# Performance work log

Measured on AMD Instinct MI355X. Metric: run time of the kernel, lower is better.

The kernel has to match this reference:

```python
import jax, jax.numpy as jnp
import numpy as np

V, E, H, HC = 20000, 300, 512, 256
B, N, LE, NW, LW, NC, LC = 16, 64, 16, 8, 16, 64, 16


def _gru_dir(xg, W_hh, b_hh, reverse):
    # xg: [B, T, 3*Hc] precomputed input gates; returns final hidden [B, Hc]
    xs = jnp.swapaxes(xg, 0, 1)
    if reverse:
        xs = xs[::-1]
    h0 = jnp.zeros((xg.shape[0], W_hh.shape[1]), xg.dtype)

    def step(h, xt):
        hr, hz, hn = jnp.split(h @ W_hh.T + b_hh, 3, axis=-1)
        xr, xz, xn = jnp.split(xt, 3, axis=-1)
        r = jax.nn.sigmoid(xr + hr)
        z = jax.nn.sigmoid(xz + hz)
        n = jnp.tanh(xn + r * hn)
        return (1.0 - z) * n + z * h, None

    hT, _ = jax.lax.scan(step, h0, xs)
    return hT


def _bigru(x, Wif, Whf, bif, bhf, Wib, Whb, bib, bhb):
    # x: [B, T, D] -> concat(fwd final, bwd final) = [B, 2*Hc]  (matches torch h_n.permute(1,0,2).reshape)
    hf = _gru_dir(x @ Wif.T + bif, Whf, bhf, False)
    hb = _gru_dir(x @ Wib.T + bib, Whb, bhb, True)
    return jnp.concatenate([hf, hb], axis=-1)


def setup_inputs() -> dict:
    key = jax.random.key(0)
    ks = iter(jax.random.split(key, 64))
    f = lambda *s: jax.random.normal(next(ks), s, jnp.float32) * 0.05
    ri = lambda *s: jax.random.randint(next(ks), s, 0, V)
    return {
        "emb_table": f(V, E),
        "W_prj": f(H, E),
        "dn_Wif": f(3 * HC, H), "dn_Whf": f(3 * HC, HC), "dn_bif": f(3 * HC), "dn_bhf": f(3 * HC),
        "dn_Wib": f(3 * HC, H), "dn_Whb": f(3 * HC, HC), "dn_bib": f(3 * HC), "dn_bhb": f(3 * HC),
        "W_e": f(H, H), "W_l": f(H, H), "W_w": f(H, H),
        "Wg": f(H, H), "bg": f(H),
        "diff_Wif": f(3 * H, H), "diff_Whf": f(3 * H, H), "diff_bif": f(3 * H), "diff_bhf": f(3 * H),
        "diff_Wib": f(3 * H, H), "diff_Whb": f(3 * H, H), "diff_bib": f(3 * H), "diff_bhb": f(3 * H),
        "Wc": f(1, 2 * H), "bc": f(1),
        "Wa1": f(2 * H, 2 * H), "ba1": f(2 * H), "Wa2": f(1, 2 * H), "ba2": f(1),
        "local_adj": jnp.zeros((64, 64), jnp.float32),
        "obs": ri(B, 32),
        "local_graph": ri(64, 8),
        "entities": ri(B, N, LE),
        "locals_": ri(B, N, LE),
        "worlds": ri(B, N, NW, LW),
        "commands": ri(B, NC, LC),
    }


def reference(emb_table, W_prj,
              dn_Wif, dn_Whf, dn_bif, dn_bhf, dn_Wib, dn_Whb, dn_bib, dn_bhb,
              W_e, W_l, W_w, Wg, bg,
              diff_Wif, diff_Whf, diff_bif, diff_bhf, diff_Wib, diff_Whb, diff_bib, diff_bhb,
              Wc, bc, Wa1, ba1, Wa2, ba2,
              local_adj, obs, local_graph, entities, locals_, worlds, commands):
    dn = (dn_Wif, dn_Whf, dn_bif, dn_bhf, dn_Wib, dn_Whb, dn_bib, dn_bhb)
    emb = lambda ids: emb_table[ids] @ W_prj.T  # embedding lookup + no-bias projection to H

    b, n, le = entities.shape
    ent_h = _bigru(emb(entities).reshape(b * n, le, H), *dn).reshape(b, n, H)
    ll = locals_.shape[-1]
    loc_h = _bigru(emb(locals_).reshape(b * n, ll, H), *dn).reshape(b, n, H)
    nw, lw = worlds.shape[2], worlds.shape[3]
    w_h = _bigru(emb(worlds).reshape(b * n * nw, lw, H), *dn).reshape(b, n, nw, H)
    worlds_sum = (w_h @ W_w).sum(axis=2)  # [b, n, H]

    # torch.ones(H,H) + W_e  ==  broadcastable 1.0 + W_e
    graph_hidden = jax.nn.elu(ent_h @ (1.0 + W_e)) + jax.nn.elu(loc_h @ W_l) + worlds_sum
    graph_encoding = jax.nn.elu(jax.nn.elu(graph_hidden) @ Wg.T + bg)  # graph_prj (dropout=eval identity)

    # value network: 'diff' path
    diff_h = _bigru(graph_encoding, diff_Wif, diff_Whf, diff_bif, diff_bhf,
                    diff_Wib, diff_Whb, diff_bib, diff_bhb)  # [b, 2H]
    value = (diff_h @ Wc.T + bc).reshape(b, 1, 1)

    nc, lc = commands.shape[1], commands.shape[2]
    c_h = _bigru(emb(commands).reshape(b * nc, lc, H), *dn).reshape(b, nc, H)

    rep = jnp.concatenate([
        jnp.broadcast_to(c_h[:, None, :, :], (b, n, nc, H)),
        jnp.broadcast_to(graph_encoding[:, :, None, :], (b, n, nc, H)),
    ], axis=-1)  # [b, n, nc, 2H]
    s = jax.nn.elu(rep @ Wa1.T + ba1) @ Wa2.T + ba2  # att_cmd (dropout p=0)
    scores = s[..., 0].mean(axis=1)  # mean over entities -> [b, nc]

    mask = commands.sum(axis=2) > 0
    probs = jax.nn.softmax(jnp.where(mask, scores, -1e9), axis=1)
    index = jnp.argmax(probs, axis=1).reshape(1, b, 1)  # deterministic stand-in for multinomial(1)
    return scores, index, value
```

## Files before the change

kernel.cpp:

```cpp
#include <hip/hip_runtime.h>
#include <stdint.h>

#define DEVFN __device__ __forceinline__

typedef __attribute__((ext_vector_type(4))) float fx4;
typedef __attribute__((ext_vector_type(8))) short sx8;
typedef __bf16 bf16x8 __attribute__((ext_vector_type(8)));

DEVFN float eluf(float x){ return x>0.f ? x : __expf(x)-1.f; }
DEVFN float sigm(float x){ return 1.f/(1.f+__expf(-x)); }
DEVFN float tanhf_(float x){ float cx=fminf(10.f,fmaxf(-10.f,x)); float e=__expf(-2.f*cx); return (1.f-e)/(1.f+e); }

DEVFN fx4 MFMA(sx8 a, sx8 b, fx4 c){
  return __builtin_amdgcn_mfma_f32_16x16x32_bf16(
      __builtin_bit_cast(bf16x8,a), __builtin_bit_cast(bf16x8,b), c, 0,0,0);
}
DEVFN void splitf(float x, short& hi, short& lo){
  __bf16 h = (__bf16)x; hi = __builtin_bit_cast(short, h);
  __bf16 l = (__bf16)(x - (float)h); lo = __builtin_bit_cast(short, l);
}

struct TT { const float* src; float* dst; int srows, scols, drows; };
struct TTs { TT t[4]; };
__global__ void k_prep_t(TTs ts){
  TT tk = ts.t[blockIdx.y];
  size_t tot = (size_t)tk.drows * tk.srows;
  for (size_t i = (size_t)blockIdx.x*256 + threadIdx.x; i < tot; i += (size_t)gridDim.x*256){
    int c = (int)(i / tk.srows), r = (int)(i % tk.srows);
    tk.dst[i] = (c < tk.scols) ? tk.src[(size_t)r*tk.scols + c] : 0.f;
  }
}
struct PL { const float* src; __bf16* hi; __bf16* lo; size_t n; };
struct PLs { PL t[2]; };
__global__ void k_prep_planes(PLs ts){
  PL tk = ts.t[blockIdx.y];
  for (size_t i = (size_t)blockIdx.x*256 + threadIdx.x; i < tk.n; i += (size_t)gridDim.x*256){
    float x = tk.src[i];
    __bf16 h = (__bf16)x;
    tk.hi[i] = h; tk.lo[i] = (__bf16)(x - (float)h);
  }
}
struct BC { const float* src; __bf16* dst; size_t n; };
struct BCs { BC t[2]; };
__global__ void k_prep_b16(BCs ts){
  BC tk = ts.t[blockIdx.y];
  for (size_t i = (size_t)blockIdx.x*256 + threadIdx.x; i < tk.n; i += (size_t)gridDim.x*256)
    tk.dst[i] = (__bf16)tk.src[i];
}
__global__ void k_toks(const int* __restrict__ ents, const int* __restrict__ locs,
                       const int* __restrict__ wrl, const int* __restrict__ cmd,
                       int* __restrict__ toks){
  int idx = blockIdx.x*256 + threadIdx.x;
  if (idx >= 2*16*11264) return;
  int dir = idx / (16*11264);
  int rem = idx % (16*11264);
  int s = rem / 11264, c = rem % 11264;
  const int* tp;
  if (c<1024) tp = ents + c*16;
  else if (c<2048) tp = locs + (c-1024)*16;
  else if (c<10240) tp = wrl + (c-2048)*16;
  else tp = cmd + (c-10240)*16;
  toks[idx] = tp[dir ? 15-s : s];
}
__global__ void k_cat_bias(const float* __restrict__ a, const float* __restrict__ b,
                           float* __restrict__ o){
  int i = blockIdx.x*256 + threadIdx.x;
  if (i < 768) o[i] = a[i];
  else if (i < 1536) o[i] = b[i-768];
}

template<int EPI, int OBF>
__global__ __launch_bounds__(256) void gemm_k(
    const float* __restrict__ A, const float* __restrict__ B,
    const float* __restrict__ bias, void* __restrict__ out,
    int M, int N, int Kpad, int Kreal, int lda, int ldb)
{
  int bm = blockIdx.y*64, bn = blockIdx.x*64;
  int tid = threadIdx.x, l = tid&63, w = tid>>6;
  int wm = (w>>1)*32, wn = (w&1)*32;
  int lr = l&15, lk = l>>4;
  fx4 acc[2][2] = {};
  for (int k0 = 0; k0 < Kpad; k0 += 32) {
    sx8 ahi[2], alo[2], bhi[2], blo[2];
    bool full = (k0 + 32 <= Kreal);
    #pragma unroll
    for (int i=0;i<2;i++){
      int row = bm + wm + i*16 + lr; row = row < M ? row : M-1;
      int col = bn + wn + i*16 + lr;
      const float* ap = A + (size_t)row*lda + k0 + lk*8;
      const float* bp = B + (size_t)col*ldb + k0 + lk*8;
      float av[8], bv[8];
      if (full){
        *(fx4*)av = *(const fx4*)ap; *(fx4*)(av+4) = *(const fx4*)(ap+4);
        *(fx4*)bv = *(const fx4*)bp; *(fx4*)(bv+4) = *(const fx4*)(bp+4);
      } else {
        #pragma unroll
        for (int j=0;j<8;j++){
          int k = k0 + lk*8 + j;
          av[j] = (k < Kreal) ? ap[j] : 0.f;
          bv[j] = (k < Kreal) ? bp[j] : 0.f;
        }
      }
      #pragma unroll
      for (int j=0;j<8;j++){
        short h,lo2; splitf(av[j], h, lo2); ahi[i][j]=h; alo[i][j]=lo2;
        splitf(bv[j], h, lo2); bhi[i][j]=h; blo[i][j]=lo2;
      }
    }
    #pragma unroll
    for (int i=0;i<2;i++)
      #pragma unroll
      for (int j=0;j<2;j++){
        acc[i][j] = MFMA(alo[i], bhi[j], acc[i][j]);
        acc[i][j] = MFMA(ahi[i], blo[j], acc[i][j]);
        acc[i][j] = MFMA(ahi[i], bhi[j], acc[i][j]);
      }
  }
  #pragma unroll
  for (int i=0;i<2;i++)
    #pragma unroll
    for (int j=0;j<2;j++)
      #pragma unroll
      for (int q=0;q<4;q++){
        int m = bm + wm + i*16 + lk*4 + q;
        int n = bn + wn + j*16 + lr;
        if (m < M){
          float v = acc[i][j][q];
          if (EPI>=1) v += bias[n];
          if (EPI==2) v = eluf(v);
          if (OBF) ((__bf16*)out)[(size_t)m*N + n] = (__bf16)v;
          else     ((float*)out)[(size_t)m*N + n] = v;
        }
      }
}

struct DnDir {
  const __bf16 *Hshi, *Hslo;
  __bf16 *Hdhi, *Hdlo;
  const __bf16 *Whi, *Wlo;
  const float *bias;
  const float *T;
  const int *toks;
  int tstride;
  int dircol;
};
__global__ __launch_bounds__(512) void dn_step(DnDir d0, DnDir d1,
                                               float* __restrict__ seqh, int s)
{
  int bx = blockIdx.x;
  int sel = (bx >= 176) ? 1 : 0;
  DnDir d = sel ? d1 : d0;
  int bm = (bx - sel*176)*64;
  int jbase = blockIdx.y*128;
  int tid = threadIdx.x, l = tid&63, w = tid>>6;
  int mg = (w>>2)*32;
  int jq = (w&3)*32;
  int lr = l&15, lk = l>>4;
  fx4 acc[2][2][3] = {};
  if (s > 0){
    for (int kk=0;kk<8;kk++){
      sx8 ah[2], al[2];
      #pragma unroll
      for (int i=0;i<2;i++){
        int m = bm + mg + i*16 + lr;
        ah[i] = *(const sx8*)(d.Hshi + (size_t)m*256 + kk*32 + lk*8);
        al[i] = *(const sx8*)(d.Hslo + (size_t)m*256 + kk*32 + lk*8);
      }
      #pragma unroll
      for (int jt=0;jt<2;jt++){
        #pragma unroll
        for (int role=0;role<3;role++){
          int col = role*256 + jbase + jq + jt*16 + lr;
          sx8 bhf = *(const sx8*)(d.Whi + (size_t)col*256 + kk*32 + lk*8);
          sx8 blf = *(const sx8*)(d.Wlo + (size_t)col*256 + kk*32 + lk*8);
          #pragma unroll
          for (int i=0;i<2;i++){
            fx4 a = acc[i][jt][role];
            a = MFMA(al[i], bhf, a);
            a = MFMA(ah[i], blf, a);
            a = MFMA(ah[i], bhf, a);
            acc[i][jt][role] = a;
          }
        }
      }
    }
  }
  const int* tks = d.toks + s*11264;
  #pragma unroll
  for (int i=0;i<2;i++){
    #pragma unroll
    for (int q=0;q<4;q++){
      int m = bm + mg + i*16 + lk*4 + q;
      int tok = tks[m];
      const float* trow = d.T + (size_t)tok*d.tstride;
      #pragma unroll
      for (int jt=0;jt<2;jt++){
        int j = jbase + jq + jt*16 + lr;
        float hr = acc[i][jt][0][q] + d.bias[j];
        float hz = acc[i][jt][1][q] + d.bias[256+j];
        float hn = acc[i][jt][2][q] + d.bias[512+j];
        float xr = trow[j], xz = trow[256+j], xn = trow[512+j];
        float ho = 0.f;
        if (s > 0) ho = (float)d.Hshi[(size_t)m*256+j] + (float)d.Hslo[(size_t)m*256+j];
        float r = sigm(xr+hr), z = sigm(xz+hz);
        float n = tanhf_(xn + r*hn);
        float v = (1.f-z)*n + z*ho;
        __bf16 hh = (__bf16)v;
        d.Hdhi[(size_t)m*256+j] = hh;
        d.Hdlo[(size_t)m*256+j] = (__bf16)(v - (float)hh);
        if (s == 15) seqh[(size_t)m*512 + d.dircol*256 + j] = v;
      }
    }
  }
}

__global__ void k_wsum(const float* __restrict__ seqh, float* __restrict__ ws){
  int r = blockIdx.x;
  for (int c = threadIdx.x; c < 512; c += 256){
    float a = 0.f;
    #pragma unroll
    for (int w8=0; w8<8; w8++) a += seqh[((size_t)2048 + r*8 + w8)*512 + c];
    ws[(size_t)r*512 + c] = a;
  }
}
__global__ void k_rowsum(const float* __restrict__ seqh, float* __restrict__ rs){
  int r = blockIdx.x, l = threadIdx.x;
  float a = 0.f;
  for (int c=l;c<512;c+=64) a += seqh[(size_t)r*512+c];
  #pragma unroll
  for (int o=32;o>0;o>>=1) a += __shfl_down(a,o);
  if (l==0) rs[r]=a;
}
__global__ void k_combine(const float* __restrict__ E1, const float* __restrict__ E2,
                          const float* __restrict__ E3, const float* __restrict__ rs,
                          float* __restrict__ y){
  size_t i = (size_t)blockIdx.x*256 + threadIdx.x;
  int r = (int)(i >> 9);
  float g = eluf(E1[i] + rs[r]) + eluf(E2[i]) + E3[i];
  y[i] = eluf(g);
}

__global__ __launch_bounds__(256) void diff_step(
  const float* __restrict__ hsrc, float* __restrict__ hdst,
  const __bf16* __restrict__ Whf, const __bf16* __restrict__ Whb,
  const float* __restrict__ bhf, const float* __restrict__ bhb,
  const __bf16* __restrict__ Xf, const __bf16* __restrict__ Xb, int t)
{
  int wg = blockIdx.x;
  int dir = wg>>3, seg = wg&7;
  const __bf16* W = dir? Whb: Whf;
  const float* bh = dir? bhb: bhf;
  const __bf16* X = dir? Xb: Xf;
  int tt = dir? 63-t : t;
  int tid = threadIdx.x, l = tid&63, w = tid>>6;
  int lr=l&15, lk=l>>4;
  int jbase = seg*64 + w*16;
  fx4 acc[3] = {};
  const float* hrow = hsrc + (size_t)dir*16*512;
  for (int kk=0;kk<16;kk++){
    const float* ap = hrow + (size_t)lr*512 + kk*32 + lk*8;
    float av[8];
    *(fx4*)av = *(const fx4*)ap; *(fx4*)(av+4) = *(const fx4*)(ap+4);
    sx8 ah, al;
    #pragma unroll
    for (int j=0;j<8;j++){ short h,lo; splitf(av[j],h,lo); ah[j]=h; al[j]=lo; }
    #pragma unroll
    for (int role=0;role<3;role++){
      int col = role*512 + jbase + lr;
      sx8 b = *(const sx8*)(W + (size_t)col*512 + kk*32 + lk*8);
      acc[role] = MFMA(al, b, acc[role]);
      acc[role] = MFMA(ah, b, acc[role]);
    }
  }
  #pragma unroll
  for (int q=0;q<4;q++){
    int m = lk*4+q;
    int j = jbase + lr;
    float hr = acc[0][q] + bh[j];
    float hz = acc[1][q] + bh[512+j];
    float hn = acc[2][q] + bh[1024+j];
    const __bf16* xrow = X + ((size_t)m*64 + tt)*1536;
    float xr = (float)xrow[j], xz = (float)xrow[512+j], xn = (float)xrow[1024+j];
    float ho = hrow[(size_t)m*512 + j];
    float r = sigm(xr+hr), z = sigm(xz+hz);
    float n = tanhf_(xn + r*hn);
    hdst[((size_t)dir*16 + m)*512 + j] = (1.f-z)*n + z*ho;
  }
}

__global__ __launch_bounds__(256) void k_score(
  const float* __restrict__ Amat, const float* __restrict__ Gmat,
  const float* __restrict__ Wa2, const float* __restrict__ ba2, float* __restrict__ sc)
{
  __shared__ float red[4];
  int p = blockIdx.x, b = p>>6, tid = threadIdx.x;
  float av[4], wv[4];
  #pragma unroll
  for (int k=0;k<4;k++){ av[k] = Amat[(size_t)p*1024 + tid + k*256]; wv[k] = Wa2[tid + k*256]; }
  float acc = 0.f;
  for (int n=0;n<64;n++){
    const float* g = Gmat + ((size_t)b*64+n)*1024;
    #pragma unroll
    for (int k=0;k<4;k++) acc += wv[k]*eluf(av[k] + g[tid + k*256]);
  }
  #pragma unroll
  for (int o=32;o>0;o>>=1) acc += __shfl_down(acc,o);
  if ((tid&63)==0) red[tid>>6] = acc;
  __syncthreads();
  if (tid==0) sc[p] = (red[0]+red[1]+red[2]+red[3])*(1.f/64.f) + ba2[0];
}

__global__ void k_final(const float* __restrict__ sc, const int* __restrict__ cmds,
                        const float* __restrict__ hfin, const float* __restrict__ Wc,
                        const float* __restrict__ bc, float* __restrict__ out)
{
  int b = blockIdx.x, l = threadIdx.x;
  out[b*64+l] = sc[b*64+l];
  int ssum = 0;
  const int* cr = cmds + (b*64+l)*16;
  #pragma unroll
  for (int k=0;k<16;k++) ssum += cr[k];
  float v = ssum>0 ? sc[b*64+l] : -1e9f;
  int idx = l;
  #pragma unroll
  for (int o=32;o>0;o>>=1){
    float ov = __shfl_down(v,o); int oi = __shfl_down(idx,o);
    if (ov > v || (ov==v && oi<idx)) { v=ov; idx=oi; }
  }
  if (l==0) out[1024 + b] = (float)idx;
  float a = 0.f;
  for (int j=l;j<512;j+=64) a += hfin[(size_t)b*512+j] * Wc[j];
  for (int j=l;j<512;j+=64) a += hfin[(size_t)(16+b)*512+j] * Wc[512+j];
  #pragma unroll
  for (int o=32;o>0;o>>=1) a += __shfl_down(a,o);
  if (l==0) out[1040 + b] = a + bc[0];
}

static inline void launch_gemm(hipStream_t st, const float* A, const float* B,
                               const float* bias, void* out, int M, int N,
                               int Kpad, int Kreal, int lda, int ldb, int epi, int obf)
{
  dim3 g(N/64, (M+63)/64), blk(256);
  if      (epi==0 && obf==0) gemm_k<0,0><<<g,blk,0,st>>>(A,B,bias,out,M,N,Kpad,Kreal,lda,ldb);
  else if (epi==1 && obf==0) gemm_k<1,0><<<g,blk,0,st>>>(A,B,bias,out,M,N,Kpad,Kreal,lda,ldb);
  else if (epi==2 && obf==0) gemm_k<2,0><<<g,blk,0,st>>>(A,B,bias,out,M,N,Kpad,Kreal,lda,ldb);
  else                       gemm_k<1,1><<<g,blk,0,st>>>(A,B,bias,out,M,N,Kpad,Kreal,lda,ldb);
}

extern "C" void kernel_launch(void* const* d_in, const int* in_sizes, int n_in,
                              void* d_out, int out_size, void* d_ws, size_t ws_size,
                              hipStream_t stream) {
  (void)in_sizes; (void)n_in; (void)out_size;
  const float* emb   = (const float*)d_in[0];
  const float* W_prj = (const float*)d_in[1];
  const float* dnWif = (const float*)d_in[2];
  const float* dnWhf = (const float*)d_in[3];
  const float* dnbif = (const float*)d_in[4];
  const float* dnbhf = (const float*)d_in[5];
  const float* dnWib = (const float*)d_in[6];
  const float* dnWhb = (const float*)d_in[7];
  const float* dnbib = (const float*)d_in[8];
  const float* dnbhb = (const float*)d_in[9];
  const float* W_e   = (const float*)d_in[10];
  const float* W_l   = (const float*)d_in[11];
  const float* W_w   = (const float*)d_in[12];
  const float* Wg    = (const float*)d_in[13];
  const float* bg    = (const float*)d_in[14];
  const float* dWif  = (const float*)d_in[15];
  const float* dWhf  = (const float*)d_in[16];
  const float* dbif  = (const float*)d_in[17];
  const float* dbhf  = (const float*)d_in[18];
  const float* dWib  = (const float*)d_in[19];
  const float* dWhb  = (const float*)d_in[20];
  const float* dbib  = (const float*)d_in[21];
  const float* dbhb  = (const float*)d_in[22];
  const float* Wc    = (const float*)d_in[23];
  const float* bc    = (const float*)d_in[24];
  const float* Wa1   = (const float*)d_in[25];
  const float* ba1   = (const float*)d_in[26];
  const float* Wa2   = (const float*)d_in[27];
  const float* ba2   = (const float*)d_in[28];
  const int* ents = (const int*)d_in[32];
  const int* locs = (const int*)d_in[33];
  const int* wrl  = (const int*)d_in[34];
  const int* cmds = (const int*)d_in[35];

  char* ws = (char*)d_ws;
  size_t off = 0;
#define WSP(name, type, count) type* name = (type*)(ws + off); off += (((size_t)(count))*sizeof(type) + 255) & ~(size_t)255;
  WSP(pWprjT, float, 320*512);
  WSP(pC2,    float, 1536*320);
  WSP(pB2,    float, 1536);
  WSP(pWhFhi, __bf16, 768*256);
  WSP(pWhFlo, __bf16, 768*256);
  WSP(pWhBhi, __bf16, 768*256);
  WSP(pWhBlo, __bf16, 768*256);
  WSP(pWeT,   float, 512*512);
  WSP(pWlT,   float, 512*512);
  WSP(pWwT,   float, 512*512);
  WSP(pdWhF,  __bf16, 1536*512);
  WSP(pdWhB,  __bf16, 1536*512);
  WSP(pSeqh,  float, 11264*512);
  WSP(pH0hi,  __bf16, 11264*256);
  WSP(pH0lo,  __bf16, 11264*256);
  WSP(pH1hi,  __bf16, 11264*256);
  WSP(pH1lo,  __bf16, 11264*256);
  WSP(pH2A,   __bf16, 11264*256);
  WSP(pH2B,   __bf16, 11264*256);
  WSP(pH2C,   __bf16, 11264*256);
  WSP(pH2D,   __bf16, 11264*256);
  WSP(pToks,  int,    2*16*11264);
  WSP(pHA,    float, 32*512);
  WSP(pHB,    float, 32*512);
  WSP(pRs,    float, 1024);
  WSP(pScf,   float, 1024);
#undef WSP
  __bf16* pH2hi[2] = { pH2A, pH2C };
  __bf16* pH2lo[2] = { pH2B, pH2D };
  float* pT = (float*)(ws + off);
  size_t trem = (ws_size > off) ? (ws_size - off) : 0;
  const size_t TBL = (size_t)20000*1536*sizeof(float);
  bool comb = trem >= TBL;

  const size_t SZ = (size_t)1024*512*4;
  char* sc = (char*)pT;
  float* pWsum = (float*)(sc + 0*SZ);
  float* pE1   = (float*)(sc + 1*SZ);
  float* pE2   = (float*)(sc + 2*SZ);
  float* pE3   = (float*)(sc + 3*SZ);
  float* pY    = (float*)(sc + 4*SZ);
  float* pGe   = (float*)(sc + 5*SZ);
  float* pAmat = (float*)(sc + 6*SZ);
  float* pGmat = (float*)(sc + 8*SZ);
  __bf16* pXf  = (__bf16*)(sc + 10*SZ);
  __bf16* pXb  = (__bf16*)(sc + 10*SZ + (size_t)1024*1536*2);

  TTs tt;
  tt.t[0] = { W_prj, pWprjT, 512, 300, 320 };
  tt.t[1] = { W_e,   pWeT,   512, 512, 512 };
  tt.t[2] = { W_l,   pWlT,   512, 512, 512 };
  tt.t[3] = { W_w,   pWwT,   512, 512, 512 };
  k_prep_t<<<dim3(256,4), 256, 0, stream>>>(tt);
  PLs pl;
  pl.t[0] = { dnWhf, pWhFhi, pWhFlo, (size_t)768*256 };
  pl.t[1] = { dnWhb, pWhBhi, pWhBlo, (size_t)768*256 };
  k_prep_planes<<<dim3(256,2), 256, 0, stream>>>(pl);
  BCs bcs;
  bcs.t[0] = { dWhf, pdWhF, (size_t)1536*512 };
  bcs.t[1] = { dWhb, pdWhB, (size_t)1536*512 };
  k_prep_b16<<<dim3(512,2), 256, 0, stream>>>(bcs);
  k_toks<<<1408, 256, 0, stream>>>(ents, locs, wrl, cmds, pToks);
  k_cat_bias<<<6, 256, 0, stream>>>(dnbif, dnbib, pB2);

  launch_gemm(stream, dnWif, pWprjT, nullptr, pC2,           768, 320, 512, 512, 512, 512, 0, 0);
  launch_gemm(stream, dnWib, pWprjT, nullptr, pC2 + 768*320, 768, 320, 512, 512, 512, 512, 0, 0);

  if (comb){
    launch_gemm(stream, emb, pC2, pB2, pT, 20000, 1536, 320, 300, 300, 320, 1, 0);
    for (int s = 0; s < 16; ++s){
      int pp = s & 1;
      DnDir D0 = { pp? pH1hi:pH0hi, pp? pH1lo:pH0lo,
                   pp? pH0hi:pH1hi, pp? pH0lo:pH1lo,
                   pWhFhi, pWhFlo, dnbhf, pT,       pToks,               1536, 0 };
      DnDir D1 = { pH2hi[pp], pH2lo[pp], pH2hi[pp^1], pH2lo[pp^1],
                   pWhBhi, pWhBlo, dnbhb, pT + 768, pToks + 16*11264,    1536, 1 };
      dn_step<<<dim3(352,2), 512, 0, stream>>>(D0, D1, pSeqh, s);
    }
  } else {
    for (int dir = 0; dir < 2; ++dir){
      launch_gemm(stream, emb, dir? pC2 + 768*320 : pC2, dir? dnbib : dnbif, pT,
                  20000, 768, 320, 300, 300, 320, 1, 0);
      for (int s = 0; s < 16; ++s){
        int pp = s & 1;
        DnDir D = { pp? pH1hi:pH0hi, pp? pH1lo:pH0lo,
                    pp? pH0hi:pH1hi, pp? pH0lo:pH1lo,
                    dir? pWhBhi:pWhFhi, dir? pWhBlo:pWhFlo, dir? dnbhb:dnbhf,
                    pT, pToks + (size_t)dir*16*11264, 768, dir };
        dn_step<<<dim3(176,2), 512, 0, stream>>>(D, D, pSeqh, s);
      }
    }
  }

  k_wsum<<<1024, 256, 0, stream>>>(pSeqh, pWsum);
  k_rowsum<<<1024, 64, 0, stream>>>(pSeqh, pRs);
  launch_gemm(stream, pSeqh,                   pWeT, nullptr, pE1, 1024, 512, 512, 512, 512, 512, 0, 0);
  launch_gemm(stream, pSeqh + (size_t)1024*512,pWlT, nullptr, pE2, 1024, 512, 512, 512, 512, 512, 0, 0);
  launch_gemm(stream, pWsum,                   pWwT, nullptr, pE3, 1024, 512, 512, 512, 512, 512, 0, 0);
  k_combine<<<2048, 256, 0, stream>>>(pE1, pE2, pE3, pRs, pY);
  launch_gemm(stream, pY, Wg, bg, pGe, 1024, 512, 512, 512, 512, 512, 2, 0);
  launch_gemm(stream, pGe, dWif, dbif, pXf, 1024, 1536, 512, 512, 512, 512, 1, 1);
  launch_gemm(stream, pGe, dWib, dbib, pXb, 1024, 1536, 512, 512, 512, 512, 1, 1);
  launch_gemm(stream, pSeqh + (size_t)10240*512, Wa1, nullptr, pAmat, 1024, 1024, 512, 512, 512, 1024, 0, 0);
  launch_gemm(stream, pGe, Wa1 + 512, ba1, pGmat, 1024, 1024, 512, 512, 512, 1024, 1, 0);
  k_score<<<1024, 256, 0, stream>>>(pAmat, pGmat, Wa2, ba2, pScf);
  hipMemsetAsync(pHA, 0, 32*512*sizeof(float), stream);
  float* ha = pHA; float* hb = pHB;
  for (int t=0; t<64; ++t){
    diff_step<<<16, 256, 0, stream>>>(ha, hb, pdWhF, pdWhB, dbhf, dbhb, pXf, pXb, t);
    float* tmp = ha; ha = hb; hb = tmp;
  }
  k_final<<<16, 64, 0, stream>>>(pScf, cmds, ha, Wc, bc, (float*)d_out);
}
```

Baseline: 2.965 ms.

## Fuse per-token input projection into GRU step instead of precomputing vocab table

Drops the precomputed 20000x1536 gate table (a full-vocab GEMM that most tokens never use). Instead, each recurrent step gathers the bf16 hi/lo split embeddings for its tokens and multiplies them by the folded projection on the fly with MFMA. Tiles now cover 32 rows by all 256 hidden columns per block, and workspace buffers get fixed allocations. This adds per-step input GEMM work (10 k-iterations of 3-pass MFMA) across the 16 sequential steps, in exchange for removing the large table GEMM and its memory traffic.

```diff
diff --git a/kernel.cpp b/kernel.cpp
--- a/kernel.cpp
+++ b/kernel.cpp
@@ -38,6 +38,16 @@
     float x = tk.src[i];
     __bf16 h = (__bf16)x;
     tk.hi[i] = h; tk.lo[i] = (__bf16)(x - (float)h);
+  }
+}
+__global__ void k_split(const float* __restrict__ src, __bf16* __restrict__ hi,
+                        __bf16* __restrict__ lo, int rows, int cin, int cout, int stride){
+  size_t tot = (size_t)rows * cout;
+  for (size_t i = (size_t)blockIdx.x*256 + threadIdx.x; i < tot; i += (size_t)gridDim.x*256){
+    int r = (int)(i / cout), c = (int)(i % cout);
+    float x = (c < cin) ? src[(size_t)r*stride + c] : 0.f;
+    __bf16 h = (__bf16)x;
+    hi[i] = h; lo[i] = (__bf16)(x - (float)h);
   }
 }
 struct BC { const float* src; __bf16* dst; size_t n; };
@@ -134,35 +144,64 @@
       }
 }
 
-struct DnDir {
+struct DnD {
   const __bf16 *Hshi, *Hslo;
   __bf16 *Hdhi, *Hdlo;
   const __bf16 *Whi, *Wlo;
-  const float *bias;
-  const float *T;
+  const __bf16 *Chi, *Clo;
+  const float *bH, *bX;
+  const __bf16 *Ehi, *Elo;
   const int *toks;
-  int tstride;
   int dircol;
 };
-__global__ __launch_bounds__(512) void dn_step(DnDir d0, DnDir d1,
+__global__ __launch_bounds__(512) void dn_step(DnD d0, DnD d1,
                                                float* __restrict__ seqh, int s)
 {
   int bx = blockIdx.x;
-  int sel = (bx >= 176) ? 1 : 0;
-  DnDir d = sel ? d1 : d0;
-  int bm = (bx - sel*176)*64;
-  int jbase = blockIdx.y*128;
+  int sel = (bx >= 352) ? 1 : 0;
+  DnD d = sel ? d1 : d0;
+  int cb = (bx - sel*352)*32;
   int tid = threadIdx.x, l = tid&63, w = tid>>6;
-  int mg = (w>>2)*32;
-  int jq = (w&3)*32;
+  int jq = w*32;
   int lr = l&15, lk = l>>4;
-  fx4 acc[2][2][3] = {};
+  const int* tks = d.toks + s*11264;
+  int tokA[2];
+  tokA[0] = tks[cb + lr];
+  tokA[1] = tks[cb + 16 + lr];
+  fx4 aRZ[2][2][2] = {};
+  fx4 aHn[2][2] = {};
+  fx4 aXn[2][2] = {};
+  for (int kk=0; kk<10; ++kk){
+    sx8 eh[2], el[2];
+    #pragma unroll
+    for (int i=0;i<2;i++){
+      eh[i] = *(const sx8*)(d.Ehi + (size_t)tokA[i]*320 + kk*32 + lk*8);
+      el[i] = *(const sx8*)(d.Elo + (size_t)tokA[i]*320 + kk*32 + lk*8);
+    }
+    #pragma unroll
+    for (int jt=0;jt<2;jt++){
+      #pragma unroll
+      for (int role=0;role<3;role++){
+        int col = role*256 + jq + jt*16 + lr;
+        sx8 bh_ = *(const sx8*)(d.Chi + (size_t)col*320 + kk*32 + lk*8);
+        sx8 bl_ = *(const sx8*)(d.Clo + (size_t)col*320 + kk*32 + lk*8);
+        #pragma unroll
+        for (int i=0;i<2;i++){
+          fx4 a = (role<2) ? aRZ[i][jt][role] : aXn[i][jt];
+          a = MFMA(el[i], bh_, a);
+          a = MFMA(eh[i], bl_, a);
+          a = MFMA(eh[i], bh_, a);
+          if (role<2) aRZ[i][jt][role] = a; else aXn[i][jt] = a;
+        }
+      }
+    }
+  }
   if (s > 0){
     for (int kk=0;kk<8;kk++){
       sx8 ah[2], al[2];
       #pragma unroll
       for (int i=0;i<2;i++){
-        int m = bm + mg + i*16 + lr;
+        int m = cb + i*16 + lr;
         ah[i] = *(const sx8*)(d.Hshi + (size_t)m*256 + kk*32 + lk*8);
         al[i] = *(const sx8*)(d.Hslo + (size_t)m*256 + kk*32 + lk*8);
       }
@@ -170,39 +209,35 @@
       for (int jt=0;jt<2;jt++){
         #pragma unroll
         for (int role=0;role<3;role++){
-          int col = role*256 + jbase + jq + jt*16 + lr;
-          sx8 bhf = *(const sx8*)(d.Whi + (size_t)col*256 + kk*32 + lk*8);
-          sx8 blf = *(const sx8*)(d.Wlo + (size_t)col*256 + kk*32 + lk*8);
+          int col = role*256 + jq + jt*16 + lr;
+          sx8 bh_ = *(const sx8*)(d.Whi + (size_t)col*256 + kk*32 + lk*8);
+          sx8 bl_ = *(const sx8*)(d.Wlo + (size_t)col*256 + kk*32 + lk*8);
           #pragma unroll
           for (int i=0;i<2;i++){
-            fx4 a = acc[i][jt][role];
-            a = MFMA(al[i], bhf, a);
-            a = MFMA(ah[i], blf, a);
-            a = MFMA(ah[i], bhf, a);
-            acc[i][jt][role] = a;
+            fx4 a = (role<2) ? aRZ[i][jt][role] : aHn[i][jt];
+            a = MFMA(al[i], bh_, a);
+            a = MFMA(ah[i], bl_, a);
+            a = MFMA(ah[i], bh_, a);
+            if (role<2) aRZ[i][jt][role] = a; else aHn[i][jt] = a;
           }
         }
       }
     }
   }
-  const int* tks = d.toks + s*11264;
   #pragma unroll
   for (int i=0;i<2;i++){
     #pragma unroll
     for (int q=0;q<4;q++){
-      int m = bm + mg + i*16 + lk*4 + q;
-      int tok = tks[m];
-      const float* trow = d.T + (size_t)tok*d.tstride;
+      int m = cb + i*16 + lk*4 + q;
       #pragma unroll
       for (int jt=0;jt<2;jt++){
-        int j = jbase + jq + jt*16 + lr;
-        float hr = acc[i][jt][0][q] + d.bias[j];
-        float hz = acc[i][jt][1][q] + d.bias[256+j];
-        float hn = acc[i][jt][2][q] + d.bias[512+j];
-        float xr = trow[j], xz = trow[256+j], xn = trow[512+j];
+        int j = jq + jt*16 + lr;
+        float r = sigm(aRZ[i][jt][0][q] + d.bX[j]     + d.bH[j]);
+        float z = sigm(aRZ[i][jt][1][q] + d.bX[256+j] + d.bH[256+j]);
+        float xn = aXn[i][jt][q] + d.bX[512+j];
+        float hn = aHn[i][jt][q] + d.bH[512+j];
         float ho = 0.f;
         if (s > 0) ho = (float)d.Hshi[(size_t)m*256+j] + (float)d.Hslo[(size_t)m*256+j];
-        float r = sigm(xr+hr), z = sigm(xz+hz);
         float n = tanhf_(xn + r*hn);
         float v = (1.f-z)*n + z*ho;
         __bf16 hh = (__bf16)v;
@@ -350,7 +385,7 @@
 extern "C" void kernel_launch(void* const* d_in, const int* in_sizes, int n_in,
                               void* d_out, int out_size, void* d_ws, size_t ws_size,
                               hipStream_t stream) {
-  (void)in_sizes; (void)n_in; (void)out_size;
+  (void)in_sizes; (void)n_in; (void)out_size; (void)ws_size;
   const float* emb   = (const float*)d_in[0];
   const float* W_prj = (const float*)d_in[1];
   const float* dnWif = (const float*)d_in[2];
@@ -391,6 +426,10 @@
   WSP(pWprjT, float, 320*512);
   WSP(pC2,    float, 1536*320);
   WSP(pB2,    float, 1536);
+  WSP(pEhi,   __bf16, 20000*320);
+  WSP(pElo,   __bf16, 20000*320);
+  WSP(pC2hi,  __bf16, 1536*320);
+  WSP(pC2lo,  __bf16, 1536*320);
   WSP(pWhFhi, __bf16, 768*256);
   WSP(pWhFlo, __bf16, 768*256);
   WSP(pWhBhi, __bf16, 768*256);
@@ -414,26 +453,19 @@
   WSP(pHB,    float, 32*512);
   WSP(pRs,    float, 1024);
   WSP(pScf,   float, 1024);
+  WSP(pWsum,  float, 1024*512);
+  WSP(pE1,    float, 1024*512);
+  WSP(pE2,    float, 1024*512);
+  WSP(pE3,    float, 1024*512);
+  WSP(pY,     float, 1024*512);
+  WSP(pGe,    float, 1024*512);
+  WSP(pAmat,  float, 1024*1024);
+  WSP(pGmat,  float, 1024*1024);
+  WSP(pXf,    __bf16, 1024*1536);
+  WSP(pXb,    __bf16, 1024*1536);
 #undef WSP
   __bf16* pH2hi[2] = { pH2A, pH2C };
   __bf16* pH2lo[2] = { pH2B, pH2D };
-  float* pT = (float*)(ws + off);
-  size_t trem = (ws_size > off) ? (ws_size - off) : 0;
-  const size_t TBL = (size_t)20000*1536*sizeof(float);
-  bool comb = trem >= TBL;
-
-  const size_t SZ = (size_t)1024*512*4;
-  char* sc = (char*)pT;
-  float* pWsum = (float*)(sc + 0*SZ);
-  float* pE1   = (float*)(sc + 1*SZ);
-  float* pE2   = (float*)(sc + 2*SZ);
-  float* pE3   = (float*)(sc + 3*SZ);
-  float* pY    = (float*)(sc + 4*SZ);
-  float* pGe   = (float*)(sc + 5*SZ);
-  float* pAmat = (float*)(sc + 6*SZ);
-  float* pGmat = (float*)(sc + 8*SZ);
-  __bf16* pXf  = (__bf16*)(sc + 10*SZ);
-  __bf16* pXb  = (__bf16*)(sc + 10*SZ + (size_t)1024*1536*2);
 
   TTs tt;
   tt.t[0] = { W_prj, pWprjT, 512, 300, 320 };
@@ -451,34 +483,22 @@
   k_prep_b16<<<dim3(512,2), 256, 0, stream>>>(bcs);
   k_toks<<<1408, 256, 0, stream>>>(ents, locs, wrl, cmds, pToks);
   k_cat_bias<<<6, 256, 0, stream>>>(dnbif, dnbib, pB2);
+  k_split<<<2048, 256, 0, stream>>>(emb, pEhi, pElo, 20000, 300, 320, 300);
 
   launch_gemm(stream, dnWif, pWprjT, nullptr, pC2,           768, 320, 512, 512, 512, 512, 0, 0);
   launch_gemm(stream, dnWib, pWprjT, nullptr, pC2 + 768*320, 768, 320, 512, 512, 512, 512, 0, 0);
-
-  if (comb){
-    launch_gemm(stream, emb, pC2, pB2, pT, 20000, 1536, 320, 300, 300, 320, 1, 0);
-    for (int s = 0; s < 16; ++s){
-      int pp = s & 1;
-      DnDir D0 = { pp? pH1hi:pH0hi, pp? pH1lo:pH0lo,
-                   pp? pH0hi:pH1hi, pp? pH0lo:pH1lo,
-                   pWhFhi, pWhFlo, dnbhf, pT,       pToks,               1536, 0 };
-      DnDir D1 = { pH2hi[pp], pH2lo[pp], pH2hi[pp^1], pH2lo[pp^1],
-                   pWhBhi, pWhBlo, dnbhb, pT + 768, pToks + 16*11264,    1536, 1 };
-      dn_step<<<dim3(352,2), 512, 0, stream>>>(D0, D1, pSeqh, s);
-    }
-  } else {
-    for (int dir = 0; dir < 2; ++dir){
-      launch_gemm(stream, emb, dir? pC2 + 768*320 : pC2, dir? dnbib : dnbif, pT,
-                  20000, 768, 320, 300, 300, 320, 1, 0);
-      for (int s = 0; s < 16; ++s){
-        int pp = s & 1;
-        DnDir D = { pp? pH1hi:pH0hi, pp? pH1lo:pH0lo,
-                    pp? pH0hi:pH1hi, pp? pH0lo:pH1lo,
-                    dir? pWhBhi:pWhFhi, dir? pWhBlo:pWhFlo, dir? dnbhb:dnbhf,
-                    pT, pToks + (size_t)dir*16*11264, 768, dir };
-        dn_step<<<dim3(176,2), 512, 0, stream>>>(D, D, pSeqh, s);
-      }
-    }
+  k_split<<<512, 256, 0, stream>>>(pC2, pC2hi, pC2lo, 1536, 320, 320, 320);
+
+  for (int s = 0; s < 16; ++s){
+    int pp = s & 1;
+    DnD D0 = { pp? pH1hi:pH0hi, pp? pH1lo:pH0lo,
+               pp? pH0hi:pH1hi, pp? pH0lo:pH1lo,
+               pWhFhi, pWhFlo, pC2hi, pC2lo,
+               dnbhf, pB2, pEhi, pElo, pToks, 0 };
+    DnD D1 = { pH2hi[pp], pH2lo[pp], pH2hi[pp^1], pH2lo[pp^1],
+               pWhBhi, pWhBlo, pC2hi + (size_t)768*320, pC2lo + (size_t)768*320,
+               dnbhb, pB2 + 768, pEhi, pElo, pToks + 16*11264, 1 };
+    dn_step<<<704, 512, 0, stream>>>(D0, D1, pSeqh, s);
   }
 
   k_wsum<<<1024, 256, 0, stream>>>(pSeqh, pWsum);
```

After: 4.310 ms. 1.45x slower.
